# Performance work log

Hardware: AMD Instinct MI355X
Metric: run time of the kernel (lower is better)

The kernel has to match this reference:

```python
import jax, jax.numpy as jnp
import numpy as np

N = 8192          # num_nodes
F_IN = 512        # num_features
D = 256           # embedding_dim
C = 40            # num_classes
E = 262144        # num_edges (avg degree 32)
ALPHA = 0.5
LN_EPS = 1e-5


def _layer_norm(x, eps=LN_EPS):
    # F.layer_norm over last dim, no affine params
    mu = jnp.mean(x, axis=-1, keepdims=True)
    var = jnp.var(x, axis=-1, keepdims=True)
    return (x - mu) * jax.lax.rsqrt(var + eps)


def setup_inputs() -> dict:
    key = jax.random.key(0)
    ks = jax.random.split(key, 16)
    s_in = 1.0 / np.sqrt(F_IN)
    s_d = 1.0 / np.sqrt(D)
    inp = {
        "X": jax.random.normal(ks[0], (N, F_IN), dtype=jnp.float32),
        "edge_row": jnp.sort(jax.random.randint(ks[1], (E,), 0, N)),
        "edge_col": jax.random.randint(ks[2], (E,), 0, N),
        "edge_weight": jax.random.uniform(ks[3], (E,), dtype=jnp.float32),
        # MLP embedding: Linear(F_IN, D)
        "W_emb": jax.random.uniform(ks[4], (F_IN, D), minval=-s_in, maxval=s_in),
        "b_emb": jax.random.uniform(ks[5], (D,), minval=-s_in, maxval=s_in),
        # attention projections: Linear(D, D) x3
        "W_q": jax.random.uniform(ks[6], (D, D), minval=-s_d, maxval=s_d),
        "b_q": jax.random.uniform(ks[7], (D,), minval=-s_d, maxval=s_d),
        "W_k": jax.random.uniform(ks[8], (D, D), minval=-s_d, maxval=s_d),
        "b_k": jax.random.uniform(ks[9], (D,), minval=-s_d, maxval=s_d),
        "W_v": jax.random.uniform(ks[10], (D, D), minval=-s_d, maxval=s_d),
        "b_v": jax.random.uniform(ks[11], (D,), minval=-s_d, maxval=s_d),
        # GNN linear: Linear(D, D)
        "W_gnn": jax.random.uniform(ks[12], (D, D), minval=-s_d, maxval=s_d),
        "b_gnn": jax.random.uniform(ks[13], (D,), minval=-s_d, maxval=s_d),
        # classifier: Linear(D, C)
        "W_cls": jax.random.uniform(ks[14], (D, C), minval=-s_d, maxval=s_d),
        "b_cls": jax.random.uniform(ks[15], (C,), minval=-s_d, maxval=s_d),
    }
    return inp


def reference(X, edge_row, edge_col, edge_weight,
              W_emb, b_emb, W_q, b_q, W_k, b_k, W_v, b_v,
              W_gnn, b_gnn, W_cls, b_cls):
    # embedding MLP
    Z0 = X @ W_emb + b_emb                      # [N, D]
    # global attention with QK layer-norm
    Q = _layer_norm(Z0 @ W_q + b_q)             # [N, D]
    K = _layer_norm(Z0 @ W_k + b_k)             # [N, D]
    V = Z0 @ W_v + b_v                          # [N, D]
    scores = Q @ K.T                            # [N, N]
    attn = jax.nn.softmax(scores, axis=-1)      # [N, N]
    Z_A = attn @ V                              # [N, D]
    # sparse GNN branch: spmm(A, linear(Z0))
    H = Z0 @ W_gnn + b_gnn                      # [N, D]
    msg = H[edge_col] * edge_weight[:, None]    # [E, D]
    gnn_out = jax.ops.segment_sum(msg, edge_row, num_segments=N)  # [N, D]
    # weighted blend + classifier
    Z_out = (1.0 - ALPHA) * Z_A + ALPHA * gnn_out
    Y_hat = Z_out @ W_cls + b_cls               # [N, C]
    return (Y_hat, attn)
```

## Files before the change

kernel.cpp:

```cpp
#include <hip/hip_runtime.h>
#include <hip/hip_bf16.h>

#define N_NODES 8192
#define F_IN    512
#define DIM     256
#define NCLS    40

typedef __attribute__((ext_vector_type(8))) short bf16x8;
typedef __attribute__((ext_vector_type(4))) float f32x4;

#define MFMA16 __builtin_amdgcn_mfma_f32_16x16x32_bf16

static __device__ __forceinline__ unsigned short f2bf(float x) {
    __hip_bfloat16 h = __float2bfloat16(x);
    return *reinterpret_cast<unsigned short*>(&h);
}
static __device__ __forceinline__ float bf2f(unsigned short u) {
    union { unsigned int u32; float f; } v; v.u32 = ((unsigned int)u) << 16;
    return v.f;
}
static __device__ __forceinline__ void gll16(const void* g, void* l) {
    __builtin_amdgcn_global_load_lds(
        (const __attribute__((address_space(1))) unsigned int*)g,
        (__attribute__((address_space(3))) unsigned int*)l, 16, 0, 0);
}

__global__ __launch_bounds__(256) void split_kernel(
    const float* __restrict__ X,
    unsigned short* __restrict__ Xh, unsigned short* __restrict__ Xl)
{
    const size_t i = ((size_t)blockIdx.x * 256 + threadIdx.x) * 4;
    float4 v = *(const float4*)&X[i];
    ushort4 h, l;
    h.x = f2bf(v.x); l.x = f2bf(v.x - bf2f(h.x));
    h.y = f2bf(v.y); l.y = f2bf(v.y - bf2f(h.y));
    h.z = f2bf(v.z); l.z = f2bf(v.z - bf2f(h.z));
    h.w = f2bf(v.w); l.w = f2bf(v.w - bf2f(h.w));
    *(ushort4*)&Xh[i] = h;
    *(ushort4*)&Xl[i] = l;
}

static __device__ __forceinline__ void wtrans_body(
    const float* __restrict__ W,
    unsigned short* __restrict__ WTh, unsigned short* __restrict__ WTl,
    int K, int N, int r0, int c0, float (*tile)[65])
{
    const int t = threadIdx.x;
    #pragma unroll
    for (int i = 0; i < 4; ++i) {
        int r = i * 16 + (t >> 4);
        int c = (t & 15) * 4;
        float4 v = *(const float4*)&W[(size_t)(r0 + r) * N + c0 + c];
        tile[r][c] = v.x; tile[r][c + 1] = v.y;
        tile[r][c + 2] = v.z; tile[r][c + 3] = v.w;
    }
    __syncthreads();
    #pragma unroll
    for (int i = 0; i < 4; ++i) {
        int c = i * 16 + (t >> 4);
        int r = (t & 15) * 4;
        ushort4 h, l;
        float x0 = tile[r][c],     x1 = tile[r + 1][c];
        float x2 = tile[r + 2][c], x3 = tile[r + 3][c];
        h.x = f2bf(x0); l.x = f2bf(x0 - bf2f(h.x));
        h.y = f2bf(x1); l.y = f2bf(x1 - bf2f(h.y));
        h.z = f2bf(x2); l.z = f2bf(x2 - bf2f(h.z));
        h.w = f2bf(x3); l.w = f2bf(x3 - bf2f(h.w));
        *(ushort4*)&WTh[(size_t)(c0 + c) * K + r0 + r] = h;
        *(ushort4*)&WTl[(size_t)(c0 + c) * K + r0 + r] = l;
    }
}

__global__ __launch_bounds__(256) void wtrans_kernel(
    const float* __restrict__ W,
    unsigned short* __restrict__ WTh, unsigned short* __restrict__ WTl,
    int K, int N)
{
    __shared__ float tile[64][65];
    wtrans_body(W, WTh, WTl, K, N, blockIdx.x * 64, blockIdx.y * 64, tile);
}

struct Wt4Args {
    const float* W[4];
    unsigned short* Th[4];
    unsigned short* Tl[4];
};

__global__ __launch_bounds__(256) void wtrans4_kernel(Wt4Args a)
{
    __shared__ float tile[64][65];
    const int z = blockIdx.z;
    wtrans_body(a.W[z], a.Th[z], a.Tl[z], DIM, DIM,
                blockIdx.x * 64, blockIdx.y * 64, tile);
}

template<int KDIM, int OUTMODE, int BM>
__device__ __forceinline__ void gemm3_body(
    const unsigned short* __restrict__ Ah_, const unsigned short* __restrict__ Al_,
    const unsigned short* __restrict__ Bh_, const unsigned short* __restrict__ Bl_,
    const float* __restrict__ bias,
    void* __restrict__ C0, void* __restrict__ C1,
    int m0, int n0,
    short (*Ah)[32], short (*Al)[32], short (*Bh)[32], short (*Bl)[32])
{
    constexpr int MFRAG = BM / 32;
    constexpr int ACH   = BM / 32;

    const int t = threadIdx.x, lane = t & 63, w = t >> 6;
    const int wm = w >> 1, wn = w & 1;
    const int fr = lane & 15, kb = lane >> 4;

    const unsigned short* asrc[ACH];
    const unsigned short* bsrc[4];
    char* adst[ACH];
    char* bdst[4];
    #pragma unroll
    for (int r = 0; r < ACH; ++r) {
        int c = r * 256 + t;
        int tens = c / (BM * 4), idx = c & (BM * 4 - 1);
        int row = idx >> 2, slot = idx & 3;
        asrc[r] = (tens ? Al_ : Ah_) + (size_t)(m0 + row) * KDIM + slot * 8;
        adst[r] = (char*)(tens ? &Al[0][0] : &Ah[0][0]) + idx * 16;
    }
    #pragma unroll
    for (int r = 0; r < 4; ++r) {
        int c = r * 256 + t;
        int tens = c >> 9, idx = c & 511;
        int row = idx >> 2, slot = idx & 3;
        bsrc[r] = (tens ? Bl_ : Bh_) + (size_t)(n0 + row) * KDIM + slot * 8;
        bdst[r] = (char*)(tens ? &Bl[0][0] : &Bh[0][0]) + idx * 16;
    }

    f32x4 acc[MFRAG][4] = {};

    for (int k0 = 0; k0 < KDIM; k0 += 32) {
        #pragma unroll
        for (int r = 0; r < ACH; ++r) { gll16(asrc[r], adst[r]); asrc[r] += 32; }
        #pragma unroll
        for (int r = 0; r < 4; ++r) { gll16(bsrc[r], bdst[r]); bsrc[r] += 32; }
        __syncthreads();

        bf16x8 ah[MFRAG], al[MFRAG], bh[4], bl[4];
        #pragma unroll
        for (int m = 0; m < MFRAG; ++m) {
            int row = wm * (BM / 2) + m * 16 + fr;
            ah[m] = *(const bf16x8*)&Ah[row][kb * 8];
            al[m] = *(const bf16x8*)&Al[row][kb * 8];
        }
        #pragma unroll
        for (int n = 0; n < 4; ++n) {
            int col = wn * 64 + n * 16 + fr;
            bh[n] = *(const bf16x8*)&Bh[col][kb * 8];
            bl[n] = *(const bf16x8*)&Bl[col][kb * 8];
        }
        #pragma unroll
        for (int m = 0; m < MFRAG; ++m)
            #pragma unroll
            for (int n = 0; n < 4; ++n) {
                acc[m][n] = MFMA16(ah[m], bh[n], acc[m][n], 0, 0, 0);
                acc[m][n] = MFMA16(ah[m], bl[n], acc[m][n], 0, 0, 0);
                acc[m][n] = MFMA16(al[m], bh[n], acc[m][n], 0, 0, 0);
            }
        __syncthreads();
    }

    #pragma unroll
    for (int m = 0; m < MFRAG; ++m)
        #pragma unroll
        for (int e = 0; e < 4; ++e) {
            const int row = m0 + wm * (BM / 2) + m * 16 + kb * 4 + e;
            #pragma unroll
            for (int n = 0; n < 4; ++n) {
                const int col = n0 + wn * 64 + n * 16 + fr;
                float v = acc[m][n][e] + bias[col];
                if (OUTMODE == 0) {
                    ((float*)C0)[(size_t)row * 256 + col] = v;
                } else if (OUTMODE == 1) {
                    ((unsigned short*)C0)[(size_t)row * 256 + col] = f2bf(v);
                } else {
                    unsigned short h = f2bf(v);
                    ((unsigned short*)C0)[(size_t)row * 256 + col] = h;
                    ((unsigned short*)C1)[(size_t)row * 256 + col] =
                        f2bf(v - bf2f(h));
                }
            }
        }
}

template<int KDIM, int OUTMODE, int BM>
__global__ __launch_bounds__(256, (BM == 64) ? 4 : 2) void mfma_gemm3_kernel(
    const unsigned short* __restrict__ Ah_, const unsigned short* __restrict__ Al_,
    const unsigned short* __restrict__ Bh_, const unsigned short* __restrict__ Bl_,
    const float* __restrict__ bias,
    void* __restrict__ C0, void* __restrict__ C1)
{
    __shared__ short Ah[BM][32], Al[BM][32], Bh[128][32], Bl[128][32];
    gemm3_body<KDIM, OUTMODE, BM>(Ah_, Al_, Bh_, Bl_, bias, C0, C1,
                                  blockIdx.y * BM, blockIdx.x * 128,
                                  Ah, Al, Bh, Bl);
}

struct Proj4Args {
    const unsigned short* Bh[4];
    const unsigned short* Bl[4];
    const float* bias[4];
    void* C[4];
};

__global__ __launch_bounds__(256, 2) void proj4_kernel(
    const unsigned short* __restrict__ Ah_, const unsigned short* __restrict__ Al_,
    Proj4Args p)
{
    __shared__ short Ah[128][32], Al[128][32], Bh[128][32], Bl[128][32];
    const int z = blockIdx.z;
    if (z < 3)
        gemm3_body<DIM, 0, 128>(Ah_, Al_, p.Bh[z], p.Bl[z], p.bias[z], p.C[z],
                                nullptr, blockIdx.y * 128, blockIdx.x * 128,
                                Ah, Al, Bh, Bl);
    else
        gemm3_body<DIM, 1, 128>(Ah_, Al_, p.Bh[z], p.Bl[z], p.bias[z], p.C[z],
                                nullptr, blockIdx.y * 128, blockIdx.x * 128,
                                Ah, Al, Bh, Bl);
}

__global__ __launch_bounds__(256) void ln_split2_kernel(
    const float* __restrict__ Qf, const float* __restrict__ Kf,
    unsigned short* __restrict__ Qh, unsigned short* __restrict__ Ql,
    unsigned short* __restrict__ Kh, unsigned short* __restrict__ Kl)
{
    const int row = blockIdx.x;
    const int t = threadIdx.x;
    const float* X = blockIdx.y ? Kf : Qf;
    unsigned short* Hi = blockIdx.y ? Kh : Qh;
    unsigned short* Lo = blockIdx.y ? Kl : Ql;

    float x = X[(size_t)row * DIM + t];

    float s1 = x, s2 = x * x;
    #pragma unroll
    for (int o = 32; o; o >>= 1) {
        s1 += __shfl_xor(s1, o);
        s2 += __shfl_xor(s2, o);
    }
    __shared__ float r1[4], r2[4];
    const int wid = t >> 6;
    if ((t & 63) == 0) { r1[wid] = s1; r2[wid] = s2; }
    __syncthreads();
    const float sum = r1[0] + r1[1] + r1[2] + r1[3];
    const float ssq = r2[0] + r2[1] + r2[2] + r2[3];
    const float mean = sum * (1.0f / DIM);
    const float var  = ssq * (1.0f / DIM) - mean * mean;
    const float y = (x - mean) * rsqrtf(var + 1e-5f);

    const unsigned short h = f2bf(y);
    Hi[(size_t)row * DIM + t] = h;
    Lo[(size_t)row * DIM + t] = f2bf(y - bf2f(h));
}

__global__ __launch_bounds__(256) void vtrans_kernel(
    const float* __restrict__ V, unsigned short* __restrict__ VT)
{
    __shared__ float tile[64][65];
    const int r0 = blockIdx.x * 64;
    const int c0 = blockIdx.y * 64;
    const int t = threadIdx.x;
    #pragma unroll
    for (int i = 0; i < 4; ++i) {
        int r = i * 16 + (t >> 4);
        int c = (t & 15) * 4;
        float4 v = *(const float4*)&V[(size_t)(r0 + r) * DIM + c0 + c];
        tile[r][c] = v.x; tile[r][c + 1] = v.y;
        tile[r][c + 2] = v.z; tile[r][c + 3] = v.w;
    }
    __syncthreads();
    #pragma unroll
    for (int i = 0; i < 4; ++i) {
        int c = i * 16 + (t >> 4);
        int r = (t & 15) * 4;
        ushort4 o;
        o.x = f2bf(tile[r][c]);     o.y = f2bf(tile[r + 1][c]);
        o.z = f2bf(tile[r + 2][c]); o.w = f2bf(tile[r + 3][c]);
        *(ushort4*)&VT[(size_t)(c0 + c) * N_NODES + r0 + r] = o;
    }
}

__global__ __launch_bounds__(256, 4) void qkt_kernel(
    const unsigned short* __restrict__ Qh, const unsigned short* __restrict__ Ql,
    const unsigned short* __restrict__ Kh, const unsigned short* __restrict__ Kl,
    unsigned short* __restrict__ Sb, float2* __restrict__ pstat)
{
    __shared__ short stage[4][128][32];
    __shared__ float2 ps[2][128];
    __shared__ float gmr[128];

    const int bid = blockIdx.x;
    const int x   = bid & 7;
    const int i   = bid >> 3;
    const int nbs = i >> 6;
    const int j   = i & 63;
    const int mb  = x * 8 + (j & 7);
    const int nb  = nbs * 8 + (j >> 3);
    const int m0 = mb * 128, n0 = nb * 128;
    const int sbbase = (nb >> 4) * 4096 + 2048 + (nb & 15) * 128;

    const int t = threadIdx.x, lane = t & 63, w = t >> 6;
    const int wm = w >> 1, wn = w & 1;
    const int fr = lane & 15, kb = lane >> 4;

    const unsigned short* qsrc[2][2];
    const unsigned short* ksrc[2][2];
    char* qdst[2][2];
    char* kdst[2][2];
    #pragma unroll
    for (int r = 0; r < 2; ++r) {
        int c = r * 256 + t;
        int row = c >> 2, slot = c & 3;
        size_t ga = (size_t)(m0 + row) * DIM + slot * 8;
        size_t gb = (size_t)(n0 + row) * DIM + slot * 8;
        qsrc[r][0] = Qh + ga; qsrc[r][1] = Ql + ga;
        ksrc[r][0] = Kh + gb; ksrc[r][1] = Kl + gb;
        qdst[r][0] = (char*)&stage[0][0][0] + c * 16;
        qdst[r][1] = (char*)&stage[1][0][0] + c * 16;
        kdst[r][0] = (char*)&stage[2][0][0] + c * 16;
        kdst[r][1] = (char*)&stage[3][0][0] + c * 16;
    }

    f32x4 acc[4][4] = {};

    for (int k0 = 0; k0 < DIM; k0 += 32) {
        #pragma unroll
        for (int r = 0; r < 2; ++r) {
            gll16(qsrc[r][0], qdst[r][0]); qsrc[r][0] += 32;
            gll16(qsrc[r][1], qdst[r][1]); qsrc[r][1] += 32;
            gll16(ksrc[r][0], kdst[r][0]); ksrc[r][0] += 32;
            gll16(ksrc[r][1], kdst[r][1]); ksrc[r][1] += 32;
        }
        __syncthreads();

        bf16x8 ah[4], al[4], bh[4], bl[4];
        #pragma unroll
        for (int m = 0; m < 4; ++m) {
            int row = wm * 64 + m * 16 + fr;
            ah[m] = *(const bf16x8*)&stage[0][row][kb * 8];
            al[m] = *(const bf16x8*)&stage[1][row][kb * 8];
        }
        #pragma unroll
        for (int n = 0; n < 4; ++n) {
            int col = wn * 64 + n * 16 + fr;
            bh[n] = *(const bf16x8*)&stage[2][col][kb * 8];
            bl[n] = *(const bf16x8*)&stage[3][col][kb * 8];
        }
        #pragma unroll
        for (int m = 0; m < 4; ++m)
            #pragma unroll
            for (int n = 0; n < 4; ++n) {
                acc[m][n] = MFMA16(ah[m], bh[n], acc[m][n], 0, 0, 0);
                acc[m][n] = MFMA16(ah[m], bl[n], acc[m][n], 0, 0, 0);
                acc[m][n] = MFMA16(al[m], bh[n], acc[m][n], 0, 0, 0);
            }
        __syncthreads();
    }

    #pragma unroll
    for (int m = 0; m < 4; ++m)
        #pragma unroll
        for (int e = 0; e < 4; ++e) {
            float mx = acc[m][0][e];
            #pragma unroll
            for (int n = 1; n < 4; ++n) mx = fmaxf(mx, acc[m][n][e]);
            #pragma unroll
            for (int o = 1; o < 16; o <<= 1) mx = fmaxf(mx, __shfl_xor(mx, o));
            if (fr == 0) ps[wn][wm * 64 + m * 16 + kb * 4 + e].x = mx;
        }
    __syncthreads();
    if (t < 128) gmr[t] = fmaxf(ps[0][t].x, ps[1][t].x);
    __syncthreads();

    unsigned short* tile = (unsigned short*)&stage[0][0][0];
    #pragma unroll
    for (int m = 0; m < 4; ++m)
        #pragma unroll
        for (int e = 0; e < 4; ++e) {
            const int rl = wm * 64 + m * 16 + kb * 4 + e;
            const float g = gmr[rl];
            const int key = kb << 1;
            float se = 0.f;
            #pragma unroll
            for (int n = 0; n < 4; ++n) {
                float ev = __expf(acc[m][n][e] - g);
                se += ev;
                const int col = wn * 64 + n * 16 + fr;
                tile[rl * 128 + (((col >> 3) ^ key) << 3) + (col & 7)] =
                    f2bf(ev);
            }
            #pragma unroll
            for (int o = 1; o < 16; o <<= 1) se += __shfl_xor(se, o);
            if (fr == 0) ps[wn][rl].y = se;
        }
    __syncthreads();
    if (t < 128)
        pstat[(size_t)(m0 + t) * 64 + nb] =
            make_float2(gmr[t], ps[0][t].y + ps[1][t].y);

    #pragma unroll
    for (int p = 0; p < 8; ++p) {
        int c = p * 256 + t;
        int r = c >> 4, sl = c & 15;
        int slx = sl ^ (((r >> 2) & 3) << 1);
        *(int4*)&Sb[(size_t)(m0 + r) * 16384 + sbbase + sl * 8] =
            *(const int4*)((const char*)tile + (r * 16 + slx) * 16);
    }
}

__global__ __launch_bounds__(256) void factor_kernel(
    const float2* __restrict__ pstat, float* __restrict__ factab)
{
    const int row = blockIdx.x * 4 + (threadIdx.x >> 6);
    const int lane = threadIdx.x & 63;
    float2 v = pstat[(size_t)row * 64 + lane];
    float gm = v.x;
    #pragma unroll
    for (int o = 1; o < 64; o <<= 1) gm = fmaxf(gm, __shfl_xor(gm, o));
    float s = v.y * __expf(v.x - gm);
    #pragma unroll
    for (int o = 1; o < 64; o <<= 1) s += __shfl_xor(s, o);
    factab[(size_t)row * 64 + lane] = __expf(v.x - gm) / s;
}

__global__ __launch_bounds__(256, 2) void av_mfma_kernel(
    const unsigned short* __restrict__ Sb, const float* __restrict__ factab,
    const unsigned short* __restrict__ VT, float* __restrict__ attn,
    float* __restrict__ P0, float* __restrict__ P1,
    float* __restrict__ P2, float* __restrict__ P3)
{
    __shared__ unsigned short As[2][64][128];
    __shared__ float facsT[16][64];

    const int bid = blockIdx.x;
    const int x = bid & 7, i = bid >> 3;
    const int ks = i >> 4;
    const int rb = (i & 15) * 8 + x;
    const int r0 = rb * 64, kbase = ks * 2048, cb0 = ks * 16;
    const int t = threadIdx.x, lane = t & 63, w = t >> 6;
    const int fr = lane & 15, kb = lane >> 4;

    for (int ii = t; ii < 1024; ii += 256)
        facsT[ii >> 6][ii & 63] =
            factab[(size_t)(r0 + (ii & 63)) * 64 + cb0 + (ii >> 6)];

    const unsigned short* vb[4];
    #pragma unroll
    for (int n = 0; n < 4; ++n)
        vb[n] = VT + (size_t)(w * 64 + n * 16 + fr) * N_NODES + kbase + kb * 8;

    const unsigned short* ssrc[4];
    char* sdst[4];
    #pragma unroll
    for (int p = 0; p < 4; ++p) {
        int c = p * 256 + t;
        int rr = c >> 4, sl = c & 15;
        int slp = sl ^ (rr & 7);
        ssrc[p] = Sb + (size_t)(r0 + rr) * 16384 + ks * 4096 + 2048 + slp * 8;
        sdst[p] = (char*)&As[0][0][0] + c * 16;
    }

    #define STAGE(BUF_) do {                                                  \
        _Pragma("unroll")                                                     \
        for (int p = 0; p < 4; ++p) {                                         \
            gll16(ssrc[p], sdst[p] + (BUF_) * 16384);                         \
            ssrc[p] += 128;                                                   \
        } } while (0)

    f32x4 acc[4][4] = {};
    const f32x4 z4 = {0.f, 0.f, 0.f, 0.f};

    STAGE(0);
    __syncthreads();

    for (int s = 0; s < 16; ++s) {
        const int b = s & 1;
        if (s + 1 < 16) STAGE(b ^ 1);

        bf16x8 bb[4][4];
        #pragma unroll
        for (int ksl = 0; ksl < 4; ++ksl)
            #pragma unroll
            for (int n = 0; n < 4; ++n)
                bb[ksl][n] = *(const bf16x8*)(vb[n] + s * 128 + ksl * 32);

        const char* abase = (const char*)&As[b][0][0];
        #pragma unroll
        for (int m = 0; m < 4; ++m) {
            f32x4 sacc[4];
            {
                bf16x8 a = *(const bf16x8*)(abase + (m * 16 + fr) * 256 +
                                            ((kb ^ (fr & 7)) * 16));
                #pragma unroll
                for (int n = 0; n < 4; ++n)
                    sacc[n] = MFMA16(a, bb[0][n], z4, 0, 0, 0);
            }
            #pragma unroll
            for (int ksl = 1; ksl < 4; ++ksl) {
                bf16x8 a = *(const bf16x8*)(abase + (m * 16 + fr) * 256 +
                                            (((ksl * 4 + kb) ^ (fr & 7)) * 16));
                #pragma unroll
                for (int n = 0; n < 4; ++n)
                    sacc[n] = MFMA16(a, bb[ksl][n], sacc[n], 0, 0, 0);
            }
            f32x4 fac = *(const f32x4*)&facsT[s][m * 16 + kb * 4];
            #pragma unroll
            for (int n = 0; n < 4; ++n)
                acc[m][n] += fac * sacc[n];
        }

        #pragma unroll
        for (int p = 0; p < 4; ++p) {
            int ci = p * 256 + t;
            int rr = ci >> 4, g = ci & 15;
            const float fac = facsT[s][rr];
            int4 v = *(const int4*)(abase + (rr * 16 + (g ^ (rr & 7))) * 16);
            float* dst = attn + (size_t)(r0 + rr) * N_NODES +
                         kbase + s * 128 + g * 8;
            float4 o0, o1;
            o0.x = bf2f((unsigned short)(v.x & 0xffff)) * fac;
            o0.y = bf2f((unsigned short)((unsigned)v.x >> 16)) * fac;
            o0.z = bf2f((unsigned short)(v.y & 0xffff)) * fac;
            o0.w = bf2f((unsigned short)((unsigned)v.y >> 16)) * fac;
            o1.x = bf2f((unsigned short)(v.z & 0xffff)) * fac;
            o1.y = bf2f((unsigned short)((unsigned)v.z >> 16)) * fac;
            o1.z = bf2f((unsigned short)(v.w & 0xffff)) * fac;
            o1.w = bf2f((unsigned short)((unsigned)v.w >> 16)) * fac;
            *(float4*)dst       = o0;
            *(float4*)(dst + 4) = o1;
        }
        __syncthreads();
    }
    #undef STAGE

    float* P = (ks == 0) ? P0 : (ks == 1) ? P1 : (ks == 2) ? P2 : P3;
    #pragma unroll
    for (int m = 0; m < 4; ++m)
        #pragma unroll
        for (int e = 0; e < 4; ++e) {
            int row = r0 + m * 16 + kb * 4 + e;
            #pragma unroll
            for (int n = 0; n < 4; ++n)
                P[(size_t)row * DIM + w * 64 + n * 16 + fr] = acc[m][n][e];
        }
}

__global__ __launch_bounds__(256) void spmm_kernel(
    const unsigned short* __restrict__ Hb, const int* __restrict__ erow,
    const int* __restrict__ ecol, const float* __restrict__ ew,
    float* __restrict__ out, int E)
{
    const int node = blockIdx.x * 4 + (threadIdx.x >> 6);
    const int lane = threadIdx.x & 63;

    int lo = 0, hi = E;
    while (lo < hi) { int mid = (lo + hi) >> 1; if (erow[mid] < node) lo = mid + 1; else hi = mid; }
    const int beg = lo;
    hi = E;
    while (lo < hi) { int mid = (lo + hi) >> 1; if (erow[mid] < node + 1) lo = mid + 1; else hi = mid; }
    const int end = lo;

    float4 acc = make_float4(0.f, 0.f, 0.f, 0.f);
    for (int e = beg; e < end; ++e) {
        const int col = ecol[e];
        const float wgt = ew[e];
        ushort4 h = *(const ushort4*)&Hb[(size_t)col * DIM + lane * 4];
        acc.x += wgt * bf2f(h.x);
        acc.y += wgt * bf2f(h.y);
        acc.z += wgt * bf2f(h.z);
        acc.w += wgt * bf2f(h.w);
    }
    *(float4*)&out[(size_t)node * DIM + lane * 4] = acc;
}

__global__ __launch_bounds__(256) void blend_cls_kernel(
    const float* __restrict__ p0, const float* __restrict__ p1,
    const float* __restrict__ p2, const float* __restrict__ p3,
    const float* __restrict__ gnn,
    const float* __restrict__ Wc, const float* __restrict__ bc,
    float* __restrict__ Y)
{
    const int row = blockIdx.x;
    const int t = threadIdx.x;
    __shared__ float z[DIM];
    __shared__ float part[4][NCLS];

    const size_t i = (size_t)row * DIM + t;
    z[t] = 0.5f * (p0[i] + p1[i] + p2[i] + p3[i] + gnn[i]);
    __syncthreads();

    if (t < 160) {
        const int c = t % NCLS, q = t / NCLS;
        float acc = 0.0f;
        #pragma unroll 4
        for (int d = q * 64; d < q * 64 + 64; ++d)
            acc += z[d] * Wc[d * NCLS + c];
        part[q][c] = acc;
    }
    __syncthreads();
    if (t < NCLS)
        Y[(size_t)row * NCLS + t] =
            part[0][t] + part[1][t] + part[2][t] + part[3][t] + bc[t];
}

extern "C" void kernel_launch(void* const* d_in, const int* in_sizes, int n_in,
                              void* d_out, int out_size, void* d_ws, size_t ws_size,
                              hipStream_t stream)
{
    const float* X     = (const float*)d_in[0];
    const int*   erow  = (const int*)d_in[1];
    const int*   ecol  = (const int*)d_in[2];
    const float* ew    = (const float*)d_in[3];
    const float* W_emb = (const float*)d_in[4];
    const float* b_emb = (const float*)d_in[5];
    const float* W_q   = (const float*)d_in[6];
    const float* b_q   = (const float*)d_in[7];
    const float* W_k   = (const float*)d_in[8];
    const float* b_k   = (const float*)d_in[9];
    const float* W_v   = (const float*)d_in[10];
    const float* b_v   = (const float*)d_in[11];
    const float* W_g   = (const float*)d_in[12];
    const float* b_g   = (const float*)d_in[13];
    const float* W_c   = (const float*)d_in[14];
    const float* b_c   = (const float*)d_in[15];
    const int E = in_sizes[1];

    float* Y    = (float*)d_out;
    float* Sc   = Y + (size_t)N_NODES * NCLS;
    unsigned short* Sb = (unsigned short*)Sc;

    const size_t ND = (size_t)N_NODES * DIM;
    float* R0 = (float*)d_ws;
    float* R1 = R0 + ND;
    float* R2 = R1 + ND;
    float* R3 = R2 + ND;
    float* R4 = R3 + ND;
    float* R5 = R4 + ND;
    float* R6 = R5 + ND;

    unsigned short* Xh = (unsigned short*)R0;
    unsigned short* Xl = (unsigned short*)R1;
    unsigned short* Wt = (unsigned short*)R2;
    unsigned short* WembTh = Wt;
    unsigned short* WembTl = Wt + 256 * 512;
    unsigned short* WqTh = WembTl + 256 * 512;
    unsigned short* WqTl = WqTh + 256 * 256;
    unsigned short* WkTh = WqTl + 256 * 256;
    unsigned short* WkTl = WkTh + 256 * 256;
    unsigned short* WvTh = WkTl + 256 * 256;
    unsigned short* WvTl = WvTh + 256 * 256;
    unsigned short* WgTh = WvTl + 256 * 256;
    unsigned short* WgTl = WgTh + 256 * 256;
    unsigned short* Z0h = (unsigned short*)R3;
    unsigned short* Z0l = Z0h + ND;
    float* Qf = R4;
    float* Kf = R5;
    float* Vf = R6;
    unsigned short* Hb = (unsigned short*)R0;
    unsigned short* Qh = (unsigned short*)R1;
    unsigned short* Ql = Qh + ND;
    unsigned short* Kh = (unsigned short*)R2;
    unsigned short* Kl = Kh + ND;
    unsigned short* VT = (unsigned short*)(R0 + ND / 2);
    float2* pstat = (float2*)R4;
    float*  factab = R5;
    float* P0 = R6;
    float* P1 = R3;
    float* P2 = R4;
    float* P3 = R1;
    float* GNN = R2;

    split_kernel<<<(N_NODES * F_IN) / 1024, 256, 0, stream>>>(X, Xh, Xl);

    wtrans_kernel<<<dim3(F_IN / 64, DIM / 64), 256, 0, stream>>>(
        W_emb, WembTh, WembTl, F_IN, DIM);
    Wt4Args wa;
    wa.W[0] = W_q; wa.Th[0] = WqTh; wa.Tl[0] = WqTl;
    wa.W[1] = W_k; wa.Th[1] = WkTh; wa.Tl[1] = WkTl;
    wa.W[2] = W_v; wa.Th[2] = WvTh; wa.Tl[2] = WvTl;
    wa.W[3] = W_g; wa.Th[3] = WgTh; wa.Tl[3] = WgTl;
    wtrans4_kernel<<<dim3(DIM / 64, DIM / 64, 4), 256, 0, stream>>>(wa);

    mfma_gemm3_kernel<F_IN, 2, 64><<<dim3(2, N_NODES / 64), 256, 0, stream>>>(
        Xh, Xl, WembTh, WembTl, b_emb, Z0h, Z0l);

    Proj4Args pa;
    pa.Bh[0] = WqTh; pa.Bl[0] = WqTl; pa.bias[0] = b_q; pa.C[0] = Qf;
    pa.Bh[1] = WkTh; pa.Bl[1] = WkTl; pa.bias[1] = b_k; pa.C[1] = Kf;
    pa.Bh[2] = WvTh; pa.Bl[2] = WvTl; pa.bias[2] = b_v; pa.C[2] = Vf;
    pa.Bh[3] = WgTh; pa.Bl[3] = WgTl; pa.bias[3] = b_g; pa.C[3] = Hb;
    proj4_kernel<<<dim3(2, N_NODES / 128, 4), 256, 0, stream>>>(Z0h, Z0l, pa);

    ln_split2_kernel<<<dim3(N_NODES, 2), 256, 0, stream>>>(
        Qf, Kf, Qh, Ql, Kh, Kl);

    vtrans_kernel<<<dim3(N_NODES / 64, DIM / 64), 256, 0, stream>>>(Vf, VT);

    qkt_kernel<<<4096, 256, 0, stream>>>(Qh, Ql, Kh, Kl, Sb, pstat);

    factor_kernel<<<N_NODES / 4, 256, 0, stream>>>(pstat, factab);

    av_mfma_kernel<<<512, 256, 0, stream>>>(
        Sb, factab, VT, Sc, P0, P1, P2, P3);

    spmm_kernel<<<N_NODES / 4, 256, 0, stream>>>(Hb, erow, ecol, ew, GNN, E);

    blend_cls_kernel<<<N_NODES, 256, 0, stream>>>(
        P0, P1, P2, P3, GNN, W_c, b_c, Y);
}
```

Baseline: 402.6 us.

## Fuse softmax factor into AV kernel and split warps into MFMA and attn-store roles

Result: no change. 402.8 us, median of 3 (+0.0%).

```diff
diff --git a/kernel.cpp b/kernel.cpp
--- a/kernel.cpp
+++ b/kernel.cpp
@@ -412,23 +412,8 @@
     }
 }
 
-__global__ __launch_bounds__(256) void factor_kernel(
-    const float2* __restrict__ pstat, float* __restrict__ factab)
-{
-    const int row = blockIdx.x * 4 + (threadIdx.x >> 6);
-    const int lane = threadIdx.x & 63;
-    float2 v = pstat[(size_t)row * 64 + lane];
-    float gm = v.x;
-    #pragma unroll
-    for (int o = 1; o < 64; o <<= 1) gm = fmaxf(gm, __shfl_xor(gm, o));
-    float s = v.y * __expf(v.x - gm);
-    #pragma unroll
-    for (int o = 1; o < 64; o <<= 1) s += __shfl_xor(s, o);
-    factab[(size_t)row * 64 + lane] = __expf(v.x - gm) / s;
-}
-
-__global__ __launch_bounds__(256, 2) void av_mfma_kernel(
-    const unsigned short* __restrict__ Sb, const float* __restrict__ factab,
+__global__ __launch_bounds__(512, 2) void av_mfma_kernel(
+    const unsigned short* __restrict__ Sb, const float2* __restrict__ pstat,
     const unsigned short* __restrict__ VT, float* __restrict__ attn,
     float* __restrict__ P0, float* __restrict__ P1,
     float* __restrict__ P2, float* __restrict__ P3)
@@ -441,12 +426,40 @@
     const int ks = i >> 4;
     const int rb = (i & 15) * 8 + x;
     const int r0 = rb * 64, kbase = ks * 2048, cb0 = ks * 16;
-    const int t = threadIdx.x, lane = t & 63, w = t >> 6;
+    const int t = threadIdx.x;
+    const bool producer = (t < 256);
+    const int tp = t & 255;
+    const int lane = tp & 63, w = tp >> 6;
     const int fr = lane & 15, kb = lane >> 4;
 
-    for (int ii = t; ii < 1024; ii += 256)
-        facsT[ii >> 6][ii & 63] =
-            factab[(size_t)(r0 + (ii & 63)) * 64 + cb0 + (ii >> 6)];
+    {
+        const int row = t >> 3;
+        const int sub = t & 7;
+        const float2* pp = pstat + (size_t)(r0 + row) * 64 + sub * 8;
+        float m = -3.0e38f, s = 0.f;
+        #pragma unroll
+        for (int jj = 0; jj < 8; ++jj) {
+            float2 v = pp[jj];
+            float nm = fmaxf(m, v.x);
+            s = s * __expf(m - nm) + v.y * __expf(v.x - nm);
+            m = nm;
+        }
+        #pragma unroll
+        for (int o = 1; o < 8; o <<= 1) {
+            float om = __shfl_xor(m, o);
+            float os = __shfl_xor(s, o);
+            float nm = fmaxf(m, om);
+            s = s * __expf(m - nm) + os * __expf(om - nm);
+            m = nm;
+        }
+        const float inv = 1.0f / s;
+        #pragma unroll
+        for (int jj = 0; jj < 2; ++jj) {
+            int cb = sub * 2 + jj;
+            float2 v = pstat[(size_t)(r0 + row) * 64 + cb0 + cb];
+            facsT[cb][row] = __expf(v.x - m) * inv;
+        }
+    }
 
     const unsigned short* vb[4];
     #pragma unroll
@@ -457,7 +470,7 @@
     char* sdst[4];
     #pragma unroll
     for (int p = 0; p < 4; ++p) {
-        int c = p * 256 + t;
+        int c = p * 256 + tp;
         int rr = c >> 4, sl = c & 15;
         int slp = sl ^ (rr & 7);
         ssrc[p] = Sb + (size_t)(r0 + rr) * 16384 + ks * 4096 + 2048 + slp * 8;
@@ -474,79 +487,84 @@
     f32x4 acc[4][4] = {};
     const f32x4 z4 = {0.f, 0.f, 0.f, 0.f};
 
-    STAGE(0);
+    if (producer) STAGE(0);
     __syncthreads();
 
     for (int s = 0; s < 16; ++s) {
         const int b = s & 1;
-        if (s + 1 < 16) STAGE(b ^ 1);
-
-        bf16x8 bb[4][4];
-        #pragma unroll
-        for (int ksl = 0; ksl < 4; ++ksl)
-            #pragma unroll
-            for (int n = 0; n < 4; ++n)
-                bb[ksl][n] = *(const bf16x8*)(vb[n] + s * 128 + ksl * 32);
-
         const char* abase = (const char*)&As[b][0][0];
-        #pragma unroll
-        for (int m = 0; m < 4; ++m) {
-            f32x4 sacc[4];
-            {
-                bf16x8 a = *(const bf16x8*)(abase + (m * 16 + fr) * 256 +
-                                            ((kb ^ (fr & 7)) * 16));
+
+        if (producer) {
+            if (s + 1 < 16) STAGE(b ^ 1);
+
+            bf16x8 bb[4][4];
+            #pragma unroll
+            for (int ksl = 0; ksl < 4; ++ksl)
                 #pragma unroll
                 for (int n = 0; n < 4; ++n)
-                    sacc[n] = MFMA16(a, bb[0][n], z4, 0, 0, 0);
-            }
-            #pragma unroll
-            for (int ksl = 1; ksl < 4; ++ksl) {
-                bf16x8 a = *(const bf16x8*)(abase + (m * 16 + fr) * 256 +
-                                            (((ksl * 4 + kb) ^ (fr & 7)) * 16));
+                    bb[ksl][n] = *(const bf16x8*)(vb[n] + s * 128 + ksl * 32);
+
+            #pragma unroll
+            for (int m = 0; m < 4; ++m) {
+                f32x4 sacc[4];
+                {
+                    bf16x8 a = *(const bf16x8*)(abase + (m * 16 + fr) * 256 +
+                                                ((kb ^ (fr & 7)) * 16));
+                    #pragma unroll
+                    for (int n = 0; n < 4; ++n)
+                        sacc[n] = MFMA16(a, bb[0][n], z4, 0, 0, 0);
+                }
+                #pragma unroll
+                for (int ksl = 1; ksl < 4; ++ksl) {
+                    bf16x8 a = *(const bf16x8*)(abase + (m * 16 + fr) * 256 +
+                                                (((ksl * 4 + kb) ^ (fr & 7)) * 16));
+                    #pragma unroll
+                    for (int n = 0; n < 4; ++n)
+                        sacc[n] = MFMA16(a, bb[ksl][n], sacc[n], 0, 0, 0);
+                }
+                f32x4 fac = *(const f32x4*)&facsT[s][m * 16 + kb * 4];
                 #pragma unroll
                 for (int n = 0; n < 4; ++n)
-                    sacc[n] = MFMA16(a, bb[ksl][n], sacc[n], 0, 0, 0);
+                    acc[m][n] += fac * sacc[n];
             }
-            f32x4 fac = *(const f32x4*)&facsT[s][m * 16 + kb * 4];
-            #pragma unroll
-            for (int n = 0; n < 4; ++n)
-                acc[m][n] += fac * sacc[n];
-        }
-
-        #pragma unroll
-        for (int p = 0; p < 4; ++p) {
-            int ci = p * 256 + t;
-            int rr = ci >> 4, g = ci & 15;
-            const float fac = facsT[s][rr];
-            int4 v = *(const int4*)(abase + (rr * 16 + (g ^ (rr & 7))) * 16);
-            float* dst = attn + (size_t)(r0 + rr) * N_NODES +
-                         kbase + s * 128 + g * 8;
-            float4 o0, o1;
-            o0.x = bf2f((unsigned short)(v.x & 0xffff)) * fac;
-            o0.y = bf2f((unsigned short)((unsigned)v.x >> 16)) * fac;
-            o0.z = bf2f((unsigned short)(v.y & 0xffff)) * fac;
-            o0.w = bf2f((unsigned short)((unsigned)v.y >> 16)) * fac;
-            o1.x = bf2f((unsigned short)(v.z & 0xffff)) * fac;
-            o1.y = bf2f((unsigned short)((unsigned)v.z >> 16)) * fac;
-            o1.z = bf2f((unsigned short)(v.w & 0xffff)) * fac;
-            o1.w = bf2f((unsigned short)((unsigned)v.w >> 16)) * fac;
-            *(float4*)dst       = o0;
-            *(float4*)(dst + 4) = o1;
+        } else {
+            #pragma unroll
+            for (int p = 0; p < 4; ++p) {
+                int ci = p * 256 + tp;
+                int rr = ci >> 4, g = ci & 15;
+                const float fac = facsT[s][rr];
+                int4 v = *(const int4*)(abase + (rr * 16 + (g ^ (rr & 7))) * 16);
+                float* dst = attn + (size_t)(r0 + rr) * N_NODES +
+                             kbase + s * 128 + g * 8;
+                float4 o0, o1;
+                o0.x = bf2f((unsigned short)(v.x & 0xffff)) * fac;
+                o0.y = bf2f((unsigned short)((unsigned)v.x >> 16)) * fac;
+                o0.z = bf2f((unsigned short)(v.y & 0xffff)) * fac;
+                o0.w = bf2f((unsigned short)((unsigned)v.y >> 16)) * fac;
+                o1.x = bf2f((unsigned short)(v.z & 0xffff)) * fac;
+                o1.y = bf2f((unsigned short)((unsigned)v.z >> 16)) * fac;
+                o1.z = bf2f((unsigned short)(v.w & 0xffff)) * fac;
+                o1.w = bf2f((unsigned short)((unsigned)v.w >> 16)) * fac;
+                *(float4*)dst       = o0;
+                *(float4*)(dst + 4) = o1;
+            }
         }
         __syncthreads();
     }
     #undef STAGE
 
-    float* P = (ks == 0) ? P0 : (ks == 1) ? P1 : (ks == 2) ? P2 : P3;
-    #pragma unroll
-    for (int m = 0; m < 4; ++m)
-        #pragma unroll
-        for (int e = 0; e < 4; ++e) {
-            int row = r0 + m * 16 + kb * 4 + e;
-            #pragma unroll
-            for (int n = 0; n < 4; ++n)
-                P[(size_t)row * DIM + w * 64 + n * 16 + fr] = acc[m][n][e];
-        }
+    if (producer) {
+        float* P = (ks == 0) ? P0 : (ks == 1) ? P1 : (ks == 2) ? P2 : P3;
+        #pragma unroll
+        for (int m = 0; m < 4; ++m)
+            #pragma unroll
+            for (int e = 0; e < 4; ++e) {
+                int row = r0 + m * 16 + kb * 4 + e;
+                #pragma unroll
+                for (int n = 0; n < 4; ++n)
+                    P[(size_t)row * DIM + w * 64 + n * 16 + fr] = acc[m][n][e];
+            }
+    }
 }
 
 __global__ __launch_bounds__(256) void spmm_kernel(
@@ -667,10 +685,9 @@
     unsigned short* Kl = Kh + ND;
     unsigned short* VT = (unsigned short*)(R0 + ND / 2);
     float2* pstat = (float2*)R4;
-    float*  factab = R5;
     float* P0 = R6;
     float* P1 = R3;
-    float* P2 = R4;
+    float* P2 = R5;
     float* P3 = R1;
     float* GNN = R2;
 
@@ -702,10 +719,8 @@
 
     qkt_kernel<<<4096, 256, 0, stream>>>(Qh, Ql, Kh, Kl, Sb, pstat);
 
-    factor_kernel<<<N_NODES / 4, 256, 0, stream>>>(pstat, factab);
-
-    av_mfma_kernel<<<512, 256, 0, stream>>>(
-        Sb, factab, VT, Sc, P0, P1, P2, P3);
+    av_mfma_kernel<<<512, 512, 0, stream>>>(
+        Sb, pstat, VT, Sc, P0, P1, P2, P3);
 
     spmm_kernel<<<N_NODES / 4, 256, 0, stream>>>(Hb, erow, ecol, ew, GNN, E);
 
```
